# Performance work log

Hardware: AMD Instinct MI355X
Metric: run time of the kernel (lower is better)

The kernel has to match this reference:

```python
import jax, jax.numpy as jnp
import numpy as np

EMBED_DIM = 1024
NUM_HEADS = 16


def setup_inputs() -> dict:
    key = jax.random.key(0)
    k_x, k_qw, k_qb, k_pw, k_bias, k_mask = jax.random.split(key, 6)
    B, N, C = 2, 2048, EMBED_DIM
    x = jax.random.normal(k_x, (B, N, C), dtype=jnp.float32)
    # torch Linear params: weight (out,in), bias (out,)
    qkv_w = jax.random.normal(k_qw, (3 * C, C), dtype=jnp.float32) * (C ** -0.5)
    qkv_b = jax.random.normal(k_qb, (3 * C,), dtype=jnp.float32) * 0.02
    proj_w = jax.random.normal(k_pw, (C, C), dtype=jnp.float32) * (C ** -0.5)
    proj_b = jnp.zeros((C,), dtype=jnp.float32)
    # nn.Parameter(torch.zeros(H,1,1)); small noise so the bias is non-trivial
    physics_bias = jax.random.normal(k_bias, (NUM_HEADS, 1, 1), dtype=jnp.float32) * 0.01
    physics_mask = jax.random.randint(k_mask, (B, 1, N, N), 0, 2).astype(jnp.int32)
    return {"x": x, "qkv_w": qkv_w, "qkv_b": qkv_b, "proj_w": proj_w,
            "proj_b": proj_b, "physics_bias": physics_bias,
            "physics_mask": physics_mask}


def reference(x, qkv_w, qkv_b, proj_w, proj_b, physics_bias, physics_mask):
    B, N, C = x.shape
    H = NUM_HEADS
    Dh = C // H
    # fused QKV projection: (B,N,3C) -> (B,N,3,H,Dh)
    qkv = (x @ qkv_w.T + qkv_b).reshape(B, N, 3, H, Dh)
    q = jnp.transpose(qkv[:, :, 0], (0, 2, 1, 3))  # (B,H,N,Dh)
    k = jnp.transpose(qkv[:, :, 1], (0, 2, 1, 3))
    v = jnp.transpose(qkv[:, :, 2], (0, 2, 1, 3))
    scale = Dh ** -0.5
    attn = jnp.einsum('bhnd,bhmd->bhnm', q, k) * scale  # (B,H,N,N)
    attn = attn + physics_bias  # (H,1,1) broadcasts per head
    attn = jnp.where(physics_mask == 0, -jnp.inf, attn)
    attn = jax.nn.softmax(attn, axis=-1)
    out = jnp.einsum('bhnm,bhmd->bhnd', attn, v)  # (B,H,N,Dh)
    out = jnp.transpose(out, (0, 2, 1, 3)).reshape(B, N, C)
    return out @ proj_w.T + proj_b
```

## Files before the change

### kernel.cpp

```cpp
#include <hip/hip_runtime.h>
#include <hip/hip_bf16.h>
#include <stdint.h>
#include <math.h>


typedef __bf16 bf16;
typedef __bf16 bf16x8 __attribute__((ext_vector_type(8)));
typedef __bf16 bf16x4 __attribute__((ext_vector_type(4)));
typedef float f32x4 __attribute__((ext_vector_type(4)));
typedef float f32x16 __attribute__((ext_vector_type(16)));

#define MFMA(a,b,c) __builtin_amdgcn_mfma_f32_16x16x32_bf16((a),(b),(c),0,0,0)
#define MFMA32(a,b,c) __builtin_amdgcn_mfma_f32_32x32x16_bf16((a),(b),(c),0,0,0)
#define L2E 1.44269504f

__device__ __forceinline__ void async16(const void* g, void* l) {
  __builtin_amdgcn_global_load_lds(
      (const __attribute__((address_space(1))) void*)g,
      (__attribute__((address_space(3))) void*)l, 16, 0, 0);
}

template <bool F32>
__device__ __forceinline__ bf16x8 ld8(const void* base, size_t off) {
  if constexpr (F32) {
    const float* p = (const float*)base + off;
    float4 u = *(const float4*)p;
    float4 v = *(const float4*)(p + 4);
    bf16x8 r;
    r[0] = (bf16)u.x; r[1] = (bf16)u.y; r[2] = (bf16)u.z; r[3] = (bf16)u.w;
    r[4] = (bf16)v.x; r[5] = (bf16)v.y; r[6] = (bf16)v.z; r[7] = (bf16)v.w;
    return r;
  } else {
    return *(const bf16x8*)((const bf16*)base + off);
  }
}

__global__ __launch_bounds__(256) void prep(const int* __restrict__ mask,
                                            unsigned long long* __restrict__ mbg,
                                            const float* __restrict__ x, bf16* __restrict__ xb,
                                            const float* __restrict__ qw, bf16* __restrict__ qwb,
                                            const float* __restrict__ pw, bf16* __restrict__ pwb) {
  int bid = blockIdx.x, tid = threadIdx.x;
  if (bid < 4096) {
    int lane = tid & 63, wv = tid >> 6;
    const int* mrow = mask + (size_t)bid * 2048;
#pragma unroll
    for (int i = 0; i < 8; ++i) {
      int w = wv * 8 + i;
      unsigned long long bal = __ballot(mrow[w * 64 + lane] != 0);
      if (lane == 0) mbg[(size_t)bid * 32 + w] = bal;
    }
  } else if (bid < 6144) {
    size_t i = ((size_t)(bid - 4096) * 256 + tid) * 8;
    *(bf16x8*)&xb[i] = ld8<true>(x, i);
  } else if (bid < 7680) {
    size_t i = ((size_t)(bid - 6144) * 256 + tid) * 8;
    *(bf16x8*)&qwb[i] = ld8<true>(qw, i);
  } else {
    size_t i = ((size_t)(bid - 7680) * 256 + tid) * 8;
    *(bf16x8*)&pwb[i] = ld8<true>(pw, i);
  }
}

template <bool AF32, bool BF32>
__device__ __forceinline__ void gemm_core(const void* __restrict__ A,
                                          const void* __restrict__ B,
                                          int m0, int n0,
                                          f32x4 acc[4][4],
                                          bf16* Al, bf16* Bl) {
  const int K = 1024;
  int tid = threadIdx.x, lane = tid & 63, wv = tid >> 6;
  int wm = wv & 1, wn = wv >> 1, g = lane >> 4, li = lane & 15;
  int r8 = lane >> 3, c8 = lane & 7;

  for (int kt = 0; kt < K; kt += 64) {
    if constexpr (!AF32 && !BF32) {
      const bf16* Ab = (const bf16*)A;
      const bf16* Bb = (const bf16*)B;
      __syncthreads();
#pragma unroll
      for (int i2 = 0; i2 < 4; ++i2) {
        int rb = wv * 32 + i2 * 8;
        async16(&Ab[(size_t)(m0 + rb + r8) * K + kt + c8 * 8], &Al[rb * 64]);
        async16(&Bb[(size_t)(n0 + rb + r8) * K + kt + c8 * 8], &Bl[rb * 64]);
      }
      __syncthreads();
    } else {
      bf16x8 ta[4], tb[4];
#pragma unroll
      for (int i2 = 0; i2 < 4; ++i2) {
        int row = wv * 32 + i2 * 8 + r8;
        ta[i2] = ld8<AF32>(A, (size_t)(m0 + row) * K + kt + c8 * 8);
        tb[i2] = ld8<BF32>(B, (size_t)(n0 + row) * K + kt + c8 * 8);
      }
      __syncthreads();
#pragma unroll
      for (int i2 = 0; i2 < 4; ++i2) {
        int row = wv * 32 + i2 * 8 + r8;
        *(bf16x8*)&Al[row * 64 + c8 * 8] = ta[i2];
        *(bf16x8*)&Bl[row * 64 + c8 * 8] = tb[i2];
      }
      __syncthreads();
    }
#pragma unroll
    for (int ks = 0; ks < 64; ks += 32) {
      bf16x8 af[4], bg[4];
#pragma unroll
      for (int i = 0; i < 4; ++i)
        af[i] = *(const bf16x8*)&Al[(wm * 64 + i * 16 + li) * 64 + ks + g * 8];
#pragma unroll
      for (int j = 0; j < 4; ++j)
        bg[j] = *(const bf16x8*)&Bl[(wn * 64 + j * 16 + li) * 64 + ks + g * 8];
#pragma unroll
      for (int i = 0; i < 4; ++i)
#pragma unroll
        for (int j = 0; j < 4; ++j)
          acc[i][j] = MFMA(af[i], bg[j], acc[i][j]);
    }
  }
}

__device__ __forceinline__ void epi_qk(f32x4 acc[4][4], int m0, int n0,
                                       const float* __restrict__ bias,
                                       bf16* __restrict__ qg, bf16* __restrict__ kg) {
  int lane = threadIdx.x & 63, wv = threadIdx.x >> 6;
  int wm = wv & 1, wn = wv >> 1, g = lane >> 4, li = lane & 15;
#pragma unroll
  for (int i = 0; i < 4; ++i) {
    int o = m0 + wm * 64 + i * 16 + g * 4;
    int s = o >> 10, h = (o >> 6) & 15, d = o & 63;
    float sc = s ? 1.0f : 0.125f * L2E;
    float b0 = bias[o], b1 = bias[o + 1], b2 = bias[o + 2], b3 = bias[o + 3];
    bf16* dstb = s ? kg : qg;
#pragma unroll
    for (int j = 0; j < 4; ++j) {
      int t = n0 + wn * 64 + j * 16 + li;
      int b = t >> 11, n = t & 2047;
      ushort4 pk;
      ((bf16*)&pk)[0] = (bf16)((acc[i][j][0] + b0) * sc);
      ((bf16*)&pk)[1] = (bf16)((acc[i][j][1] + b1) * sc);
      ((bf16*)&pk)[2] = (bf16)((acc[i][j][2] + b2) * sc);
      ((bf16*)&pk)[3] = (bf16)((acc[i][j][3] + b3) * sc);
      *(ushort4*)&dstb[(((size_t)b * 16 + h) * 2048 + n) * 64 + d] = pk;
    }
  }
}

__device__ __forceinline__ void epi_v(f32x4 acc[4][4], int m0, int n0,
                                      const float* __restrict__ bias,
                                      bf16* __restrict__ vtg) {
  int lane = threadIdx.x & 63, wvv = threadIdx.x >> 6;
  int wm = wvv & 1, wn = wvv >> 1, g = lane >> 4, li = lane & 15;
#pragma unroll
  for (int i = 0; i < 4; ++i) {
    int t = m0 + wm * 64 + i * 16 + g * 4;
    int b = t >> 11, n = t & 2047;
#pragma unroll
    for (int j = 0; j < 4; ++j) {
      int ov = n0 + wn * 64 + j * 16 + li;
      int h = ov >> 6, d = ov & 63;
      float bv = bias[ov];
      ushort4 pk;
      ((bf16*)&pk)[0] = (bf16)(acc[i][j][0] + bv);
      ((bf16*)&pk)[1] = (bf16)(acc[i][j][1] + bv);
      ((bf16*)&pk)[2] = (bf16)(acc[i][j][2] + bv);
      ((bf16*)&pk)[3] = (bf16)(acc[i][j][3] + bv);
      *(ushort4*)&vtg[(((size_t)b * 16 + h) * 64 + d) * 2048 + n] = pk;
    }
  }
}

__global__ __launch_bounds__(256) void gemm_qkv(const bf16* __restrict__ xb,
                                                const bf16* __restrict__ qwb,
                                                const float* __restrict__ bias,
                                                bf16* __restrict__ qg,
                                                bf16* __restrict__ kg,
                                                bf16* __restrict__ vtg) {
  __shared__ bf16 Al[128 * 64], Bl[128 * 64];
  f32x4 acc[4][4];
#pragma unroll
  for (int i = 0; i < 4; ++i)
#pragma unroll
    for (int j = 0; j < 4; ++j) acc[i][j] = (f32x4){0.f, 0.f, 0.f, 0.f};
  int bid = blockIdx.x;
  if (bid < 512) {
    int m0 = (bid >> 5) * 128, n0 = (bid & 31) * 128;
    gemm_core<false, false>(qwb, xb, m0, n0, acc, Al, Bl);
    epi_qk(acc, m0, n0, bias, qg, kg);
  } else {
    int vb = bid - 512;
    int m0 = (vb >> 3) * 128, n0 = (vb & 7) * 128;
    gemm_core<false, false>(xb, qwb + (size_t)2048 * 1024, m0, n0, acc, Al, Bl);
    epi_v(acc, m0, n0, bias + 2048, vtg);
  }
}

__global__ __launch_bounds__(256) void gemm_qk_f(const float* __restrict__ x,
                                                 const float* __restrict__ w,
                                                 const float* __restrict__ bias,
                                                 bf16* __restrict__ qg,
                                                 bf16* __restrict__ kg) {
  __shared__ bf16 Al[128 * 64], Bl[128 * 64];
  f32x4 acc[4][4];
#pragma unroll
  for (int i = 0; i < 4; ++i)
#pragma unroll
    for (int j = 0; j < 4; ++j) acc[i][j] = (f32x4){0.f, 0.f, 0.f, 0.f};
  int m0 = blockIdx.y * 128, n0 = blockIdx.x * 128;
  gemm_core<true, true>(w, x, m0, n0, acc, Al, Bl);
  epi_qk(acc, m0, n0, bias, qg, kg);
}
__global__ __launch_bounds__(256) void gemm_v_f(const float* __restrict__ x,
                                                const float* __restrict__ wv_,
                                                const float* __restrict__ bias,
                                                bf16* __restrict__ vtg) {
  __shared__ bf16 Al[128 * 64], Bl[128 * 64];
  f32x4 acc[4][4];
#pragma unroll
  for (int i = 0; i < 4; ++i)
#pragma unroll
    for (int j = 0; j < 4; ++j) acc[i][j] = (f32x4){0.f, 0.f, 0.f, 0.f};
  int m0 = blockIdx.y * 128, n0 = blockIdx.x * 128;
  gemm_core<true, true>(x, wv_, m0, n0, acc, Al, Bl);
  epi_v(acc, m0, n0, bias, vtg);
}
__global__ __launch_bounds__(256) void mask_bits(const int* __restrict__ mask,
                                                 unsigned long long* __restrict__ mbg) {
  int row = blockIdx.x, lane = threadIdx.x & 63, wv = threadIdx.x >> 6;
  const int* mrow = mask + (size_t)row * 2048;
#pragma unroll
  for (int i = 0; i < 8; ++i) {
    int w = wv * 8 + i;
    unsigned long long bal = __ballot(mrow[w * 64 + lane] != 0);
    if (lane == 0) mbg[(size_t)row * 32 + w] = bal;
  }
}

__global__ __launch_bounds__(256, 3) void flash_attn(
    const bf16* __restrict__ qg, const bf16* __restrict__ kg,
    const bf16* __restrict__ vtg, const unsigned long long* __restrict__ mbg,
    bf16* __restrict__ G) {
  __shared__ bf16 Kl[64 * 64];
  __shared__ bf16 Vl[64 * 64];
  __shared__ bf16 Ol[4][32 * 72];

  int tid = threadIdx.x, lane = tid & 63, wv = tid >> 6;
  int cl = lane & 31, hi = lane >> 5;
  int r8 = lane >> 3, c8 = lane & 7;
  int q0 = blockIdx.x * 128;
  int bh = blockIdx.y, b = bh >> 4;
  const bf16* qbase = qg + (size_t)bh * 2048 * 64;
  const bf16* kbase = kg + (size_t)bh * 2048 * 64;
  const bf16* vbase = vtg + (size_t)bh * 64 * 2048;

  int qrow = q0 + wv * 32 + cl;
  bf16x8 qf[4];
#pragma unroll
  for (int kd = 0; kd < 4; ++kd)
    qf[kd] = *(const bf16x8*)&qbase[(size_t)qrow * 64 + kd * 16 + hi * 8];
  const unsigned long long* mrow = mbg + (size_t)(b * 2048 + qrow) * 32;

  f32x16 accO0, accO1;
#pragma unroll
  for (int e = 0; e < 16; ++e) { accO0[e] = 0.f; accO1[e] = 0.f; }
  float lsum = 0.f;

  int srow0 = wv * 16 + r8, srow1 = wv * 16 + 8 + r8;
  int sw0 = (srow0 & 7) << 4, sw1 = (srow1 & 7) << 4;
  int ve0 = ((c8 >> 1) * 16 + (c8 & 1) * 4) * 2;
  int ve1 = ve0 + 16;
  int swr = (cl & 7) << 4;

  bf16x8 tk0 = *(const bf16x8*)&kbase[(size_t)srow0 * 64 + c8 * 8];
  bf16x8 tk1 = *(const bf16x8*)&kbase[(size_t)srow1 * 64 + c8 * 8];
  bf16x8 tv0 = *(const bf16x8*)&vbase[(size_t)srow0 * 2048 + c8 * 8];
  bf16x8 tv1 = *(const bf16x8*)&vbase[(size_t)srow1 * 2048 + c8 * 8];
  unsigned long long mw = mrow[0];

  for (int it = 0; it < 32; ++it) {
    unsigned long long mwc = mw;
    __syncthreads();
    {
      *(bf16x8*)((char*)Kl + srow0 * 128 + ((c8 * 16) ^ sw0)) = tk0;
      *(bf16x8*)((char*)Kl + srow1 * 128 + ((c8 * 16) ^ sw1)) = tk1;
      bf16x4 lo, hh;
#pragma unroll
      for (int r = 0; r < 4; ++r) { lo[r] = tv0[r]; hh[r] = tv0[r + 4]; }
      *(bf16x4*)((char*)Vl + srow0 * 128 + (ve0 ^ sw0)) = lo;
      *(bf16x4*)((char*)Vl + srow0 * 128 + (ve1 ^ sw0)) = hh;
#pragma unroll
      for (int r = 0; r < 4; ++r) { lo[r] = tv1[r]; hh[r] = tv1[r + 4]; }
      *(bf16x4*)((char*)Vl + srow1 * 128 + (ve0 ^ sw1)) = lo;
      *(bf16x4*)((char*)Vl + srow1 * 128 + (ve1 ^ sw1)) = hh;
    }
    __syncthreads();

    int n1 = ((it + 1) & 31) * 64;
    tk0 = *(const bf16x8*)&kbase[(size_t)(n1 + srow0) * 64 + c8 * 8];
    tk1 = *(const bf16x8*)&kbase[(size_t)(n1 + srow1) * 64 + c8 * 8];
    tv0 = *(const bf16x8*)&vbase[(size_t)srow0 * 2048 + n1 + c8 * 8];
    tv1 = *(const bf16x8*)&vbase[(size_t)srow1 * 2048 + n1 + c8 * 8];
    mw = mrow[(it + 1) & 31];

    f32x16 accS0, accS1;
#pragma unroll
    for (int e = 0; e < 16; ++e) { accS0[e] = 0.f; accS1[e] = 0.f; }
#pragma unroll
    for (int kd = 0; kd < 4; ++kd) {
      int cb = (kd * 32 + hi * 16) ^ swr;
      bf16x8 kf0 = *(const bf16x8*)((char*)Kl + cl * 128 + cb);
      bf16x8 kf1 = *(const bf16x8*)((char*)Kl + (32 + cl) * 128 + cb);
      accS0 = MFMA32(kf0, qf[kd], accS0);
      accS1 = MFMA32(kf1, qf[kd], accS1);
    }

    unsigned dw[16];
#pragma unroll
    for (int nb = 0; nb < 2; ++nb) {
      unsigned mql = (unsigned)(mwc >> (nb * 32));
#pragma unroll
      for (int j = 0; j < 4; ++j) {
        float s0 = nb ? accS1[4 * j + 0] : accS0[4 * j + 0];
        float s1 = nb ? accS1[4 * j + 1] : accS0[4 * j + 1];
        float s2 = nb ? accS1[4 * j + 2] : accS0[4 * j + 2];
        float s3 = nb ? accS1[4 * j + 3] : accS0[4 * j + 3];
        unsigned m4 = (mql >> (j * 8 + hi * 4)) & 0xFu;
        float p0 = (m4 & 1u) ? exp2f(s0) : 0.f;
        float p1 = (m4 & 2u) ? exp2f(s1) : 0.f;
        float p2 = (m4 & 4u) ? exp2f(s2) : 0.f;
        float p3 = (m4 & 8u) ? exp2f(s3) : 0.f;
        lsum += (p0 + p1) + (p2 + p3);
        unsigned lo2, hi2;
        ((bf16*)&lo2)[0] = (bf16)p0; ((bf16*)&lo2)[1] = (bf16)p1;
        ((bf16*)&hi2)[0] = (bf16)p2; ((bf16*)&hi2)[1] = (bf16)p3;
        dw[nb * 8 + 2 * j] = lo2;
        dw[nb * 8 + 2 * j + 1] = hi2;
      }
    }

#pragma unroll
    for (int kk = 0; kk < 4; ++kk) {
      union { unsigned u[4]; bf16x8 v; } pa;
#pragma unroll
      for (int t = 0; t < 4; ++t) pa.u[t] = dw[kk * 4 + t];
      int cb = (kk * 32 + hi * 16) ^ swr;
      bf16x8 vf0 = *(const bf16x8*)((char*)Vl + cl * 128 + cb);
      bf16x8 vf1 = *(const bf16x8*)((char*)Vl + (32 + cl) * 128 + cb);
      accO0 = MFMA32(vf0, pa.v, accO0);
      accO1 = MFMA32(vf1, pa.v, accO1);
    }
  }

  float ltot = lsum + __shfl_xor(lsum, 32);
  float inv = 1.0f / fmaxf(ltot, 1e-37f);
#pragma unroll
  for (int e = 0; e < 16; ++e) { accO0[e] *= inv; accO1[e] *= inv; }

  bf16* ow = Ol[wv];
#pragma unroll
  for (int db = 0; db < 2; ++db) {
#pragma unroll
    for (int jq = 0; jq < 4; ++jq) {
      ushort4 pk;
      ((bf16*)&pk)[0] = (bf16)(db ? accO1[4 * jq + 0] : accO0[4 * jq + 0]);
      ((bf16*)&pk)[1] = (bf16)(db ? accO1[4 * jq + 1] : accO0[4 * jq + 1]);
      ((bf16*)&pk)[2] = (bf16)(db ? accO1[4 * jq + 2] : accO0[4 * jq + 2]);
      ((bf16*)&pk)[3] = (bf16)(db ? accO1[4 * jq + 3] : accO0[4 * jq + 3]);
      int dbase = db * 32 + jq * 8 + hi * 4;
      *(ushort4*)&ow[cl * 72 + dbase] = pk;
    }
  }

  int ql = lane >> 1, part = lane & 1;
  size_t tok = (size_t)b * 2048 + q0 + wv * 32 + ql;
  bf16* dst = G + tok * 1024 + (bh & 15) * 64 + part * 32;
  const bf16* src = &ow[ql * 72 + part * 32];
#pragma unroll
  for (int j = 0; j < 4; ++j)
    *(bf16x8*)&dst[j * 8] = *(const bf16x8*)&src[j * 8];
}

__global__ __launch_bounds__(256) void gemm_proj_n(const bf16* __restrict__ G,
                                                   const bf16* __restrict__ w,
                                                   const float* __restrict__ bias,
                                                   float* __restrict__ out) {
  __shared__ bf16 Al[128 * 64], Bl[64 * 64];
  const int K = 1024;
  int tid = threadIdx.x, lane = tid & 63, wv = tid >> 6;
  int wm = wv & 1, wn = wv >> 1, g = lane >> 4, li = lane & 15;
  int r8 = lane >> 3, c8 = lane & 7;
  int m0 = blockIdx.y * 128, n0 = blockIdx.x * 64;

  f32x4 acc[4][2];
#pragma unroll
  for (int i = 0; i < 4; ++i)
#pragma unroll
    for (int j = 0; j < 2; ++j) acc[i][j] = (f32x4){0.f, 0.f, 0.f, 0.f};

  for (int kt = 0; kt < K; kt += 64) {
    __syncthreads();
#pragma unroll
    for (int i2 = 0; i2 < 4; ++i2) {
      int rb = wv * 32 + i2 * 8;
      async16(&w[(size_t)(m0 + rb + r8) * K + kt + c8 * 8], &Al[rb * 64]);
    }
#pragma unroll
    for (int i2 = 0; i2 < 2; ++i2) {
      int rb = wv * 16 + i2 * 8;
      async16(&G[(size_t)(n0 + rb + r8) * K + kt + c8 * 8], &Bl[rb * 64]);
    }
    __syncthreads();
#pragma unroll
    for (int ks = 0; ks < 64; ks += 32) {
      bf16x8 af[4], bg[2];
#pragma unroll
      for (int i = 0; i < 4; ++i)
        af[i] = *(const bf16x8*)&Al[(wm * 64 + i * 16 + li) * 64 + ks + g * 8];
#pragma unroll
      for (int j = 0; j < 2; ++j)
        bg[j] = *(const bf16x8*)&Bl[(wn * 32 + j * 16 + li) * 64 + ks + g * 8];
#pragma unroll
      for (int i = 0; i < 4; ++i)
#pragma unroll
        for (int j = 0; j < 2; ++j)
          acc[i][j] = MFMA(af[i], bg[j], acc[i][j]);
    }
  }

#pragma unroll
  for (int i = 0; i < 4; ++i) {
    int ch = m0 + wm * 64 + i * 16 + g * 4;
    float b0 = bias[ch], b1 = bias[ch + 1], b2 = bias[ch + 2], b3 = bias[ch + 3];
#pragma unroll
    for (int j = 0; j < 2; ++j) {
      int t = n0 + wn * 32 + j * 16 + li;
      float4 pk = make_float4(acc[i][j][0] + b0, acc[i][j][1] + b1,
                              acc[i][j][2] + b2, acc[i][j][3] + b3);
      *(float4*)&out[(size_t)t * 1024 + ch] = pk;
    }
  }
}

__global__ __launch_bounds__(256) void gemm_proj_f(const bf16* __restrict__ G,
                                                   const float* __restrict__ w,
                                                   const float* __restrict__ bias,
                                                   float* __restrict__ out) {
  __shared__ bf16 Al[128 * 64], Bl[128 * 64];
  f32x4 acc[4][4];
#pragma unroll
  for (int i = 0; i < 4; ++i)
#pragma unroll
    for (int j = 0; j < 4; ++j) acc[i][j] = (f32x4){0.f, 0.f, 0.f, 0.f};
  int m0 = blockIdx.y * 128, n0 = blockIdx.x * 128;
  gemm_core<true, false>(w, G, m0, n0, acc, Al, Bl);

  int lane = threadIdx.x & 63, wv = threadIdx.x >> 6;
  int wm = wv & 1, wn = wv >> 1, g = lane >> 4, li = lane & 15;
#pragma unroll
  for (int i = 0; i < 4; ++i) {
    int ch = m0 + wm * 64 + i * 16 + g * 4;
    float b0 = bias[ch], b1 = bias[ch + 1], b2 = bias[ch + 2], b3 = bias[ch + 3];
#pragma unroll
    for (int j = 0; j < 4; ++j) {
      int t = n0 + wn * 64 + j * 16 + li;
      float4 pk = make_float4(acc[i][j][0] + b0, acc[i][j][1] + b1,
                              acc[i][j][2] + b2, acc[i][j][3] + b3);
      *(float4*)&out[(size_t)t * 1024 + ch] = pk;
    }
  }
}

extern "C" void kernel_launch(void* const* d_in, const int* in_sizes, int n_in,
                              void* d_out, int out_size, void* d_ws, size_t ws_size,
                              hipStream_t stream) {
  const float* x      = (const float*)d_in[0];
  const float* qkv_w  = (const float*)d_in[1];
  const float* qkv_b  = (const float*)d_in[2];
  const float* proj_w = (const float*)d_in[3];
  const float* proj_b = (const float*)d_in[4];
  const int* mask     = (const int*)d_in[6];
  float* out = (float*)d_out;

  const size_t MB = (size_t)1 << 20;
  char* ws = (char*)d_ws;
  bf16* qg  = (bf16*)(ws);
  bf16* kg  = (bf16*)(ws + 8 * MB);
  bf16* vtg = (bf16*)(ws + 16 * MB);
  bf16* xb  = (bf16*)(ws + 24 * MB);
  bf16* G   = (bf16*)(ws + 24 * MB);
  unsigned long long* mbg = (unsigned long long*)(ws + 32 * MB);
  bf16* qwb = (bf16*)(ws + 33 * MB);
  bf16* pwb = (bf16*)(ws + 39 * MB);
  bool pre = ws_size >= 41 * MB;

  if (pre) {
    prep<<<dim3(8192), dim3(256), 0, stream>>>(mask, mbg, x, xb, qkv_w, qwb,
                                               proj_w, pwb);
    gemm_qkv<<<dim3(768), dim3(256), 0, stream>>>(xb, qwb, qkv_b, qg, kg, vtg);
  } else {
    mask_bits<<<dim3(4096), dim3(256), 0, stream>>>(mask, mbg);
    gemm_qk_f<<<dim3(32, 16), dim3(256), 0, stream>>>(x, qkv_w, qkv_b, qg, kg);
    gemm_v_f<<<dim3(8, 32), dim3(256), 0, stream>>>(
        x, qkv_w + (size_t)2048 * 1024, qkv_b + 2048, vtg);
  }

  flash_attn<<<dim3(16, 32), dim3(256), 0, stream>>>(qg, kg, vtg, mbg, G);

  if (pre)
    gemm_proj_n<<<dim3(64, 8), dim3(256), 0, stream>>>(G, pwb, proj_b, out);
  else
    gemm_proj_f<<<dim3(32, 8), dim3(256), 0, stream>>>(G, proj_w, proj_b, out);
}
```

Measured before the change: 252.2 us.

## Split attention KV loop across two wave groups and merge partial outputs

Doubles the flash-attention block to 512 threads. Two groups of four waves each process alternating 64-key tiles for the same 128 queries, each group with its own K/V shared buffers. The partial output accumulators and row sums are then combined through shared memory before normalisation. This is meant to raise wave-level parallelism and latency hiding per query tile, at the cost of more shared memory per block, an extra reduction step, and half the waves idling during the epilogue. The exp2f call is also swapped for the raw hardware exp2 builtin.

```diff
diff --git a/kernel.cpp b/kernel.cpp
--- a/kernel.cpp
+++ b/kernel.cpp
@@ -13,6 +13,12 @@
 #define MFMA(a,b,c) __builtin_amdgcn_mfma_f32_16x16x32_bf16((a),(b),(c),0,0,0)
 #define MFMA32(a,b,c) __builtin_amdgcn_mfma_f32_32x32x16_bf16((a),(b),(c),0,0,0)
 #define L2E 1.44269504f
+
+#if __has_builtin(__builtin_amdgcn_exp2f)
+#define EXP2(x) __builtin_amdgcn_exp2f(x)
+#else
+#define EXP2(x) exp2f(x)
+#endif
 
 __device__ __forceinline__ void async16(const void* g, void* l) {
   __builtin_amdgcn_global_load_lds(
@@ -236,15 +242,14 @@
   }
 }
 
-__global__ __launch_bounds__(256, 3) void flash_attn(
+__global__ __launch_bounds__(512, 4) void flash_attn(
     const bf16* __restrict__ qg, const bf16* __restrict__ kg,
     const bf16* __restrict__ vtg, const unsigned long long* __restrict__ mbg,
     bf16* __restrict__ G) {
-  __shared__ bf16 Kl[64 * 64];
-  __shared__ bf16 Vl[64 * 64];
-  __shared__ bf16 Ol[4][32 * 72];
-
-  int tid = threadIdx.x, lane = tid & 63, wv = tid >> 6;
+  __shared__ __align__(16) char smem[51712];
+
+  int tid = threadIdx.x, lane = tid & 63, wv8 = tid >> 6;
+  int grp = wv8 >> 2, wg = wv8 & 3;
   int cl = lane & 31, hi = lane >> 5;
   int r8 = lane >> 3, c8 = lane & 7;
   int q0 = blockIdx.x * 128;
@@ -252,8 +257,10 @@
   const bf16* qbase = qg + (size_t)bh * 2048 * 64;
   const bf16* kbase = kg + (size_t)bh * 2048 * 64;
   const bf16* vbase = vtg + (size_t)bh * 64 * 2048;
-
-  int qrow = q0 + wv * 32 + cl;
+  bf16* Kl = (bf16*)(smem + grp * 16384);
+  bf16* Vl = (bf16*)(smem + grp * 16384 + 8192);
+
+  int qrow = q0 + wg * 32 + cl;
   bf16x8 qf[4];
 #pragma unroll
   for (int kd = 0; kd < 4; ++kd)
@@ -265,19 +272,21 @@
   for (int e = 0; e < 16; ++e) { accO0[e] = 0.f; accO1[e] = 0.f; }
   float lsum = 0.f;
 
-  int srow0 = wv * 16 + r8, srow1 = wv * 16 + 8 + r8;
+  int srow0 = wg * 16 + r8, srow1 = wg * 16 + 8 + r8;
   int sw0 = (srow0 & 7) << 4, sw1 = (srow1 & 7) << 4;
   int ve0 = ((c8 >> 1) * 16 + (c8 & 1) * 4) * 2;
   int ve1 = ve0 + 16;
   int swr = (cl & 7) << 4;
 
-  bf16x8 tk0 = *(const bf16x8*)&kbase[(size_t)srow0 * 64 + c8 * 8];
-  bf16x8 tk1 = *(const bf16x8*)&kbase[(size_t)srow1 * 64 + c8 * 8];
-  bf16x8 tv0 = *(const bf16x8*)&vbase[(size_t)srow0 * 2048 + c8 * 8];
-  bf16x8 tv1 = *(const bf16x8*)&vbase[(size_t)srow1 * 2048 + c8 * 8];
-  unsigned long long mw = mrow[0];
-
-  for (int it = 0; it < 32; ++it) {
+  int nf = grp * 64;
+  bf16x8 tk0 = *(const bf16x8*)&kbase[(size_t)(nf + srow0) * 64 + c8 * 8];
+  bf16x8 tk1 = *(const bf16x8*)&kbase[(size_t)(nf + srow1) * 64 + c8 * 8];
+  bf16x8 tv0 = *(const bf16x8*)&vbase[(size_t)srow0 * 2048 + nf + c8 * 8];
+  bf16x8 tv1 = *(const bf16x8*)&vbase[(size_t)srow1 * 2048 + nf + c8 * 8];
+  unsigned long long mw = mrow[grp];
+
+  for (int t = 0; t < 16; ++t) {
+    int it = 2 * t + grp;
     unsigned long long mwc = mw;
     __syncthreads();
     {
@@ -295,12 +304,12 @@
     }
     __syncthreads();
 
-    int n1 = ((it + 1) & 31) * 64;
+    int n1 = ((it + 2) & 31) * 64;
     tk0 = *(const bf16x8*)&kbase[(size_t)(n1 + srow0) * 64 + c8 * 8];
     tk1 = *(const bf16x8*)&kbase[(size_t)(n1 + srow1) * 64 + c8 * 8];
     tv0 = *(const bf16x8*)&vbase[(size_t)srow0 * 2048 + n1 + c8 * 8];
     tv1 = *(const bf16x8*)&vbase[(size_t)srow1 * 2048 + n1 + c8 * 8];
-    mw = mrow[(it + 1) & 31];
+    mw = mrow[(it + 2) & 31];
 
     f32x16 accS0, accS1;
 #pragma unroll
@@ -325,10 +334,10 @@
         float s2 = nb ? accS1[4 * j + 2] : accS0[4 * j + 2];
         float s3 = nb ? accS1[4 * j + 3] : accS0[4 * j + 3];
         unsigned m4 = (mql >> (j * 8 + hi * 4)) & 0xFu;
-        float p0 = (m4 & 1u) ? exp2f(s0) : 0.f;
-        float p1 = (m4 & 2u) ? exp2f(s1) : 0.f;
-        float p2 = (m4 & 4u) ? exp2f(s2) : 0.f;
-        float p3 = (m4 & 8u) ? exp2f(s3) : 0.f;
+        float p0 = (m4 & 1u) ? EXP2(s0) : 0.f;
+        float p1 = (m4 & 2u) ? EXP2(s1) : 0.f;
+        float p2 = (m4 & 4u) ? EXP2(s2) : 0.f;
+        float p3 = (m4 & 8u) ? EXP2(s3) : 0.f;
         lsum += (p0 + p1) + (p2 + p3);
         unsigned lo2, hi2;
         ((bf16*)&lo2)[0] = (bf16)p0; ((bf16*)&lo2)[1] = (bf16)p1;
@@ -342,7 +351,7 @@
     for (int kk = 0; kk < 4; ++kk) {
       union { unsigned u[4]; bf16x8 v; } pa;
 #pragma unroll
-      for (int t = 0; t < 4; ++t) pa.u[t] = dw[kk * 4 + t];
+      for (int t2 = 0; t2 < 4; ++t2) pa.u[t2] = dw[kk * 4 + t2];
       int cb = (kk * 32 + hi * 16) ^ swr;
       bf16x8 vf0 = *(const bf16x8*)((char*)Vl + cl * 128 + cb);
       bf16x8 vf1 = *(const bf16x8*)((char*)Vl + (32 + cl) * 128 + cb);
@@ -352,11 +361,41 @@
   }
 
   float ltot = lsum + __shfl_xor(lsum, 32);
-  float inv = 1.0f / fmaxf(ltot, 1e-37f);
-#pragma unroll
-  for (int e = 0; e < 16; ++e) { accO0[e] *= inv; accO1[e] *= inv; }
-
-  bf16* ow = Ol[wv];
+
+  __syncthreads();
+  float* oc = (float*)(smem + wg * 8192);
+  float* lbuf = (float*)(smem + 32768);
+  int osw = (cl & 7) << 4;
+  if (grp == 1) {
+#pragma unroll
+    for (int j = 0; j < 4; ++j) {
+      f32x4 qa, qb;
+#pragma unroll
+      for (int r = 0; r < 4; ++r) { qa[r] = accO0[4 * j + r]; qb[r] = accO1[4 * j + r]; }
+      int dby = j * 32 + hi * 16;
+      *(f32x4*)((char*)oc + cl * 256 + (dby ^ osw)) = qa;
+      *(f32x4*)((char*)oc + cl * 256 + ((dby + 128) ^ osw)) = qb;
+    }
+    if (hi == 0) lbuf[wg * 32 + cl] = ltot;
+  }
+  __syncthreads();
+  if (grp == 1) return;
+
+  float lt2 = ltot + lbuf[wg * 32 + cl];
+  float inv = 1.0f / fmaxf(lt2, 1e-37f);
+#pragma unroll
+  for (int j = 0; j < 4; ++j) {
+    int dby = j * 32 + hi * 16;
+    f32x4 qa = *(const f32x4*)((char*)oc + cl * 256 + (dby ^ osw));
+    f32x4 qb = *(const f32x4*)((char*)oc + cl * 256 + ((dby + 128) ^ osw));
+#pragma unroll
+    for (int r = 0; r < 4; ++r) {
+      accO0[4 * j + r] = (accO0[4 * j + r] + qa[r]) * inv;
+      accO1[4 * j + r] = (accO1[4 * j + r] + qb[r]) * inv;
+    }
+  }
+
+  bf16* ow = (bf16*)(smem + 33280) + wg * (32 * 72);
 #pragma unroll
   for (int db = 0; db < 2; ++db) {
 #pragma unroll
@@ -372,7 +411,7 @@
   }
 
   int ql = lane >> 1, part = lane & 1;
-  size_t tok = (size_t)b * 2048 + q0 + wv * 32 + ql;
+  size_t tok = (size_t)b * 2048 + q0 + wg * 32 + ql;
   bf16* dst = G + tok * 1024 + (bh & 15) * 64 + part * 32;
   const bf16* src = &ow[ql * 72 + part * 32];
 #pragma unroll
@@ -504,7 +543,7 @@
         x, qkv_w + (size_t)2048 * 1024, qkv_b + 2048, vtg);
   }
 
-  flash_attn<<<dim3(16, 32), dim3(256), 0, stream>>>(qg, kg, vtg, mbg, G);
+  flash_attn<<<dim3(16, 32), dim3(512), 0, stream>>>(qg, kg, vtg, mbg, G);
 
   if (pre)
     gemm_proj_n<<<dim3(64, 8), dim3(256), 0, stream>>>(G, pwb, proj_b, out);
```

New measurement: 234.4 us. 1.08x faster.
